# Kernel optimization log

Hardware: AMD Instinct MI355X
Metric: run time of the kernel (lower is better)

## Reference

```python
import jax, jax.numpy as jnp
import numpy as np

G = 256       # number of graphs in batch
NPG = 400     # nodes per graph (hardcoded in module)
DEG = 32      # avg degree
FIN = 400     # input feature dim
H = 64        # hidden_channels
N = G * NPG
E = G * NPG * DEG


def _glorot(key, fan_in, fan_out):
    lim = float(np.sqrt(6.0 / (fan_in + fan_out)))
    return jax.random.uniform(key, (fan_in, fan_out), jnp.float32, -lim, lim)


def setup_inputs() -> dict:
    key = jax.random.key(0)
    ks = jax.random.split(key, 12)
    x = jax.random.normal(ks[0], (N, FIN), jnp.float32)
    # intra-graph random edges, then offset by graph id so edges never cross graphs
    src = jax.random.randint(ks[1], (G, NPG * DEG), 0, NPG)
    dst = jax.random.randint(ks[2], (G, NPG * DEG), 0, NPG)
    offs = (jnp.arange(G) * NPG)[:, None]
    edge_index = jnp.stack([(src + offs).reshape(-1), (dst + offs).reshape(-1)]).astype(jnp.int32)
    edge_weight = jax.random.uniform(ks[3], (E,), jnp.float32)
    return {
        "x": x,
        "edge_index": edge_index,
        "edge_weight": edge_weight,
        "W1": _glorot(ks[4], FIN, H), "b1": jnp.zeros((H,), jnp.float32),
        "W2": _glorot(ks[5], H, H),   "b2": jnp.zeros((H,), jnp.float32),
        "W3": _glorot(ks[6], H, H),   "b3": jnp.zeros((H,), jnp.float32),
        "Wc": _glorot(ks[7], NPG * H, H), "bc": jnp.zeros((H,), jnp.float32),
        "Wl": _glorot(ks[8], H, 2),   "bl": jnp.zeros((2,), jnp.float32),
    }


def _gcn_conv(x, W, b, row, col, norm, n):
    # PyG GCNConv: out[col] += norm * (x @ W)[row]; then + bias
    h = x @ W                                   # [n, out]
    msg = norm[:, None] * h[row]                # [E+n, out] gather + scale
    return jax.ops.segment_sum(msg, col, num_segments=n) + b


def reference(x, edge_index, edge_weight, W1, b1, W2, b2, W3, b3, Wc, bc, Wl, bl):
    n = x.shape[0]
    loop = jnp.arange(n, dtype=edge_index.dtype)
    row = jnp.concatenate([edge_index[0], loop])            # sources (with self-loops)
    col = jnp.concatenate([edge_index[1], loop])            # targets
    ew = jnp.concatenate([edge_weight, jnp.ones((n,), edge_weight.dtype)])
    # symmetric normalization: deg^{-1/2}[row] * w * deg^{-1/2}[col]
    deg = jax.ops.segment_sum(ew, col, num_segments=n)
    dinv = jnp.where(deg > 0, jax.lax.rsqrt(deg), 0.0)
    norm = dinv[row] * ew * dinv[col]

    h = jax.nn.relu(_gcn_conv(x, W1, b1, row, col, norm, n))
    h = jax.nn.relu(_gcn_conv(h, W2, b2, row, col, norm, n))
    h = _gcn_conv(h, W3, b3, row, col, norm, n)
    # per-graph flatten of 400 nodes -> lincomb (vectorized form of the Python loop)
    g = h.reshape(-1, NPG * H) @ Wc + bc        # [G, H]
    # dropout p=0.5 skipped (eval mode)
    return g @ Wl + bl                          # [G, 2]
```

## Files before the change

### kernel.cpp

```cpp
#include <hip/hip_runtime.h>
#include <hip/hip_bf16.h>
#include <stdint.h>

#define G 256
#define NPG 400
#define DEG 32
#define FIN 400
#define H 64
#define NN (G*NPG)
#define EE (G*NPG*DEG)
#define EPG (NPG*DEG)
#define CPG (EPG+NPG)
#define NTILE 13
#define ATS 420
#define HTS 72
#define MTSZ 25600

#define W1F_OFF 0
#define W1F_N   (13*4*64*8)
#define W2F_OFF (W1F_OFF + W1F_N)
#define W2F_N   (2*4*64*8)
#define W3F_OFF (W2F_OFF + W2F_N)
#define WCF_OFF (W3F_OFF + W2F_N)
#define WCF_N   (800*4*64*8)
#define WF_TOT  (WCF_OFF + WCF_N)

typedef __attribute__((ext_vector_type(8))) _Float16 h8;
typedef __attribute__((ext_vector_type(4))) float f32x4;

static __device__ __forceinline__ unsigned packh2(float a, float b) {
  unsigned short ua = __builtin_bit_cast(unsigned short, (_Float16)a);
  unsigned short ub = __builtin_bit_cast(unsigned short, (_Float16)b);
  return (unsigned)ua | ((unsigned)ub << 16);
}

static __device__ __forceinline__ h8 cvt8(float4 a, float4 b) {
  h8 r;
  r[0] = (_Float16)a.x; r[1] = (_Float16)a.y; r[2] = (_Float16)a.z; r[3] = (_Float16)a.w;
  r[4] = (_Float16)b.x; r[5] = (_Float16)b.y; r[6] = (_Float16)b.z; r[7] = (_Float16)b.w;
  return r;
}

__global__ __launch_bounds__(256) void kNorm(
    const int* __restrict__ ei, const float* __restrict__ ew,
    uint2* __restrict__ ent, uint32_t* __restrict__ boff)
{
  __shared__ float deg[NPG];
  __shared__ float dv[NPG];
  __shared__ uint32_t bcnt[NTILE], bpos[NTILE];
  const int g = blockIdx.x, tid = threadIdx.x;
  const int ebase = g*EPG, nbase = g*NPG;
  const int* rowp = ei;
  const int* colp = ei + EE;
  if (tid < NTILE) bcnt[tid] = 0u;
  for (int v = tid; v < NPG; v += 256) deg[v] = 1.0f;
  __syncthreads();
  for (int e = tid; e < EPG; e += 256) {
    int c = colp[ebase+e] - nbase;
    atomicAdd(&deg[c], ew[ebase+e]);
    atomicAdd(&bcnt[c >> 5], 1u);
  }
  __syncthreads();
  for (int v = tid; v < NPG; v += 256) dv[v] = rsqrtf(deg[v]);
  if (tid == 0) {
    uint32_t s = 0;
    #pragma unroll
    for (int t = 0; t < NTILE; ++t) {
      uint32_t c = bcnt[t] + ((t < 12) ? 32u : 16u);
      bcnt[t] = s; bpos[t] = s; s += c;
    }
  }
  __syncthreads();
  if (tid < NTILE) boff[g*16 + tid] = bcnt[tid];
  if (tid == NTILE) boff[g*16 + NTILE] = (uint32_t)CPG;
  uint2* eb = ent + (size_t)g*CPG;
  for (int e = tid; e < EPG; e += 256) {
    int src = rowp[ebase+e] - nbase;
    int dst = colp[ebase+e] - nbase;
    float nm = dv[src] * ew[ebase+e] * dv[dst];
    uint32_t p = atomicAdd(&bpos[dst >> 5], 1u);
    eb[p] = make_uint2(((unsigned)dst << 16) | (unsigned)src, __float_as_uint(nm));
  }
  for (int v = tid; v < NPG; v += 256) {
    uint32_t p = atomicAdd(&bpos[v >> 5], 1u);
    eb[p] = make_uint2(((unsigned)v << 16) | (unsigned)v, __float_as_uint(dv[v]*dv[v]));
  }
}

__global__ __launch_bounds__(256) void kPack(
    const float* __restrict__ W1, const float* __restrict__ W2,
    const float* __restrict__ W3, const float* __restrict__ Wc,
    _Float16* __restrict__ wf, float* __restrict__ gbuf)
{
  int idx = blockIdx.x*256 + threadIdx.x;
  if (idx < G*H) gbuf[idx] = 0.f;
  if (idx >= WF_TOT) return;
  if (idx < W2F_OFF) {
    int i = idx;
    int j = i & 7, ln = (i >> 3) & 63, nt = (i >> 9) & 3, ks = i >> 11;
    int k = ks*32 + (ln >> 4)*8 + j, col = nt*16 + (ln & 15);
    wf[idx] = (k < FIN) ? (_Float16)W1[k*H + col] : (_Float16)0.f;
  } else if (idx < W3F_OFF) {
    int i = idx - W2F_OFF;
    int j = i & 7, ln = (i >> 3) & 63, nt = (i >> 9) & 3, ks = i >> 11;
    wf[idx] = (_Float16)W2[(ks*32 + (ln >> 4)*8 + j)*H + nt*16 + (ln & 15)];
  } else if (idx < WCF_OFF) {
    int i = idx - W3F_OFF;
    int j = i & 7, ln = (i >> 3) & 63, nt = (i >> 9) & 3, ks = i >> 11;
    wf[idx] = (_Float16)W3[(ks*32 + (ln >> 4)*8 + j)*H + nt*16 + (ln & 15)];
  } else {
    int i = idx - WCF_OFF;
    int j = i & 7, ln = (i >> 3) & 63, nt = (i >> 9) & 3, kt = i >> 11;
    int kp = kt*32 + (ln >> 4)*8 + j;
    int node = kp % 400, feat = kp / 400;
    int col = nt*16 + (ln & 15);
    wf[idx] = (_Float16)Wc[((size_t)node*64 + feat)*64 + col];
  }
}

__global__ __launch_bounds__(256, 4) void kM1(
    const float* __restrict__ x, const _Float16* __restrict__ wf,
    _Float16* __restrict__ mt1)
{
  __shared__ _Float16 sh[64*HTS];
  const int tid = threadIdx.x, lane = tid & 63, wave = tid >> 6;
  const int l15 = lane & 15, kgrp = lane >> 4;
  const int g = blockIdx.y, b = blockIdx.x;
  const int node_l = b*64 + wave*16 + l15;
  const int arow = (node_l < NPG) ? node_l : NPG-1;
  const float* xp = x + ((size_t)g*NPG + arow)*FIN;

  h8 af[13];
  #pragma unroll
  for (int ks = 0; ks < 13; ++ks) {
    int kb = ks*32 + kgrp*8;
    if (kb + 8 <= FIN) {
      float4 a0 = *(const float4*)(xp + kb);
      float4 a1 = *(const float4*)(xp + kb + 4);
      af[ks] = cvt8(a0, a1);
    } else {
      h8 z;
      #pragma unroll
      for (int j = 0; j < 8; ++j) z[j] = (_Float16)0.f;
      af[ks] = z;
    }
  }
  f32x4 acc[4] = {{0,0,0,0},{0,0,0,0},{0,0,0,0},{0,0,0,0}};
  for (int nt = 0; nt < 4; ++nt)
    for (int ks = 0; ks < 13; ++ks) {
      h8 bf = *(const h8*)&wf[W1F_OFF + (((size_t)ks*4 + nt)*64 + lane)*8];
      acc[nt] = __builtin_amdgcn_mfma_f32_16x16x32_f16(af[ks], bf, acc[nt], 0, 0, 0);
    }
  #pragma unroll
  for (int nt = 0; nt < 4; ++nt) {
    int feat = nt*16 + l15;
    #pragma unroll
    for (int r = 0; r < 4; ++r)
      sh[(wave*16 + kgrp*4 + r)*HTS + feat] = (_Float16)acc[nt][r];
  }
  __syncthreads();
  const unsigned short* shu = (const unsigned short*)sh;
  for (int i = tid; i < 64*16; i += 256) {
    int feat = i >> 4, seg = i & 15;
    int nl = seg*4, gn = b*64 + nl;
    if (gn < NPG) {
      uint2 u;
      u.x = (unsigned)shu[(nl+0)*HTS + feat] | ((unsigned)shu[(nl+1)*HTS + feat] << 16);
      u.y = (unsigned)shu[(nl+2)*HTS + feat] | ((unsigned)shu[(nl+3)*HTS + feat] << 16);
      *(uint2*)&mt1[(size_t)g*MTSZ + feat*400 + gn] = u;
    }
  }
}

template<int WMUL>
__global__ __launch_bounds__(512, 4) void kAgg(
    const _Float16* __restrict__ mtin, const _Float16* __restrict__ wfn,
    const float* __restrict__ bias,
    const uint2* __restrict__ ent, const uint32_t* __restrict__ boff,
    _Float16* __restrict__ out)
{
  extern __shared__ char smem[];
  float* sAT = (float*)smem;
  _Float16* sh = (_Float16*)(smem + 32*ATS*4);
  const int tid = threadIdx.x, lane = tid & 63, wave = tid >> 6;
  const int l15 = lane & 15, kgrp = lane >> 4;
  const int bid = blockIdx.x;
  const int g = bid & 255, t = bid >> 8;
  const int t0 = t*32;
  const int rsub = wave & 1, nt = wave >> 1;
  const uint2* eb = ent + (size_t)g*CPG;
  const uint32_t s0 = boff[g*16 + t], s1 = boff[g*16 + t + 1];

  h8 BF[13];
  const _Float16* mrow = mtin + (size_t)g*MTSZ + (nt*16 + l15)*400;
  #pragma unroll
  for (int ks = 0; ks < 13; ++ks)
    BF[ks] = *(const h8*)(mrow + ks*32 + kgrp*8);
  const float bv = bias[nt*16 + l15];
  h8 WF2[2];
  if (WMUL) {
    WF2[0] = *(const h8*)&wfn[((size_t)(0*4 + nt)*64 + lane)*8];
    WF2[1] = *(const h8*)&wfn[((size_t)(1*4 + nt)*64 + lane)*8];
  }
  const uint32_t e0 = s0 + tid;
  uint2 E0 = make_uint2(0,0), E1 = make_uint2(0,0), E2 = make_uint2(0,0);
  if (e0        < s1) E0 = eb[e0];
  if (e0 + 512  < s1) E1 = eb[e0 + 512];
  if (e0 + 1024 < s1) E2 = eb[e0 + 1024];

  { float4* p = (float4*)sAT;
    for (int i = tid; i < 32*ATS/4; i += 512) p[i] = make_float4(0,0,0,0); }
  __syncthreads();

  if (e0        < s1) atomicAdd(&sAT[((int)(E0.x >> 16) - t0)*ATS + (int)(E0.x & 0xffffu)], __uint_as_float(E0.y));
  if (e0 + 512  < s1) atomicAdd(&sAT[((int)(E1.x >> 16) - t0)*ATS + (int)(E1.x & 0xffffu)], __uint_as_float(E1.y));
  if (e0 + 1024 < s1) atomicAdd(&sAT[((int)(E2.x >> 16) - t0)*ATS + (int)(E2.x & 0xffffu)], __uint_as_float(E2.y));
  for (uint32_t e = e0 + 1536; e < s1; e += 512) {
    uint2 E = eb[e];
    atomicAdd(&sAT[((int)(E.x >> 16) - t0)*ATS + (int)(E.x & 0xffffu)], __uint_as_float(E.y));
  }
  __syncthreads();

  f32x4 acc = {0,0,0,0};
  const float* ap = &sAT[(rsub*16 + l15)*ATS];
  #pragma unroll
  for (int ks = 0; ks < 13; ++ks) {
    int kb = ks*32 + kgrp*8;
    float4 a0 = *(const float4*)(ap + kb);
    float4 a1 = *(const float4*)(ap + kb + 4);
    acc = __builtin_amdgcn_mfma_f32_16x16x32_f16(cvt8(a0, a1), BF[ks], acc, 0, 0, 0);
  }

  if (!WMUL) {
    int node0 = t0 + rsub*16 + kgrp*4;
    if (node0 < NPG) {
      uint2 u;
      u.x = packh2(acc[0] + bv, acc[1] + bv);
      u.y = packh2(acc[2] + bv, acc[3] + bv);
      *(uint2*)&out[(size_t)g*MTSZ + (nt*16 + l15)*400 + node0] = u;
    }
  } else {
    int nl0 = rsub*16 + kgrp*4;
    #pragma unroll
    for (int r = 0; r < 4; ++r)
      sh[(nl0 + r)*HTS + nt*16 + l15] = (_Float16)fmaxf(acc[r] + bv, 0.f);
    __syncthreads();
    f32x4 acc2 = {0,0,0,0};
    const _Float16* hp = &sh[(rsub*16 + l15)*HTS];
    acc2 = __builtin_amdgcn_mfma_f32_16x16x32_f16(*(const h8*)(hp + kgrp*8),      WF2[0], acc2, 0, 0, 0);
    acc2 = __builtin_amdgcn_mfma_f32_16x16x32_f16(*(const h8*)(hp + 32 + kgrp*8), WF2[1], acc2, 0, 0, 0);
    int node0 = t0 + rsub*16 + kgrp*4;
    if (node0 < NPG) {
      uint2 u;
      u.x = packh2(acc2[0], acc2[1]);
      u.y = packh2(acc2[2], acc2[3]);
      *(uint2*)&out[(size_t)g*MTSZ + (nt*16 + l15)*400 + node0] = u;
    }
  }
}

__global__ __launch_bounds__(256) void kRead(
    const _Float16* __restrict__ h3, const _Float16* __restrict__ wfc,
    float* __restrict__ gbuf)
{
  const int tid = threadIdx.x, lane = tid & 63, nt = tid >> 6;
  const int l15 = lane & 15, kgrp = lane >> 4;
  const int rt = blockIdx.x & 15, kc = blockIdx.x >> 4;
  f32x4 acc = {0,0,0,0};
  const _Float16* hp = h3 + (size_t)(rt*16 + l15)*MTSZ;
  for (int ks = 0; ks < 25; ++ks) {
    int kt = kc*25 + ks;
    h8 af = *(const h8*)(hp + kt*32 + kgrp*8);
    h8 bf = *(const h8*)(wfc + (((size_t)kt*4 + nt)*64 + lane)*8);
    acc = __builtin_amdgcn_mfma_f32_16x16x32_f16(af, bf, acc, 0, 0, 0);
  }
  #pragma unroll
  for (int r = 0; r < 4; ++r)
    atomicAdd(&gbuf[(size_t)(rt*16 + kgrp*4 + r)*H + nt*16 + l15], acc[r]);
}

__global__ __launch_bounds__(512) void k6_final(
    const float* __restrict__ gbuf, const float* __restrict__ bc,
    const float* __restrict__ Wl, const float* __restrict__ bl,
    float* __restrict__ out)
{
  int t = threadIdx.x;
  int gr = t >> 1, c = t & 1;
  float acc = bl[c];
  for (int f = 0; f < H; ++f)
    acc += (gbuf[gr*H + f] + bc[f]) * Wl[f*2 + c];
  out[gr*2 + c] = acc;
}

extern "C" void kernel_launch(void* const* d_in, const int* in_sizes, int n_in,
                              void* d_out, int out_size, void* d_ws, size_t ws_size,
                              hipStream_t stream)
{
  const float* x  = (const float*)d_in[0];
  const int*   ei = (const int*)d_in[1];
  const float* ew = (const float*)d_in[2];
  const float* W1 = (const float*)d_in[3];
  const float* b1 = (const float*)d_in[4];
  const float* W2 = (const float*)d_in[5];
  const float* b2 = (const float*)d_in[6];
  const float* W3 = (const float*)d_in[7];
  const float* b3 = (const float*)d_in[8];
  const float* Wc = (const float*)d_in[9];
  const float* bc = (const float*)d_in[10];
  const float* Wl = (const float*)d_in[11];
  const float* bl = (const float*)d_in[12];
  float* out = (float*)d_out;
  (void)ws_size;

  char* ws = (char*)d_ws;
  size_t o = 0;
  uint2*     ent  = (uint2*)(ws + o);     o += (size_t)G*CPG*8;
  uint32_t*  boff = (uint32_t*)(ws + o);  o += (size_t)G*16*4;
  _Float16*  mtA  = (_Float16*)(ws + o);  o += (size_t)G*MTSZ*2 + 256;
  _Float16*  mtB  = (_Float16*)(ws + o);  o += (size_t)G*MTSZ*2 + 256;
  _Float16*  wf   = (_Float16*)(ws + o);  o += (size_t)WF_TOT*2;
  float*     gbuf = (float*)(ws + o);     o += (size_t)G*H*4;

  kPack<<<(WF_TOT+255)/256, 256, 0, stream>>>(W1, W2, W3, Wc, wf, gbuf);
  kNorm<<<G, 256, 0, stream>>>(ei, ew, ent, boff);
  kM1<<<dim3(7, G), 256, 0, stream>>>(x, wf, mtA);
  const int aggLds = 32*ATS*4 + 32*HTS*2;
  kAgg<1><<<NTILE*G, 512, aggLds, stream>>>(mtA, wf + W2F_OFF, b1, ent, boff, mtB);
  kAgg<1><<<NTILE*G, 512, aggLds, stream>>>(mtB, wf + W3F_OFF, b2, ent, boff, mtA);
  kAgg<0><<<NTILE*G, 512, aggLds, stream>>>(mtA, wf, b3, ent, boff, mtB);
  kRead<<<512, 256, 0, stream>>>(mtB, wf + WCF_OFF, gbuf);
  k6_final<<<1, 512, 0, stream>>>(gbuf, bc, Wl, bl, out);
}
```

Baseline: 290.3 us.

## Merge front-end kernels into one launch and halve aggregation tile size

Merges the normalization/CSR-bucket build, the first-layer X·W1 MFMA GEMM, and the Wc repacking into one heterogeneous kFront launch whose blocks are split by index range. W1–W3 packing stays in a separate kernel. The aggregation kernels now use 16-node destination tiles (25 tiles per graph) with 256-thread blocks, doubling the block count and halving LDS per block, which should raise occupancy. The final projection is spread across 8 blocks. This removes launches and serial dependencies between the front-end kernels, but kFront's LDS is sized only for the M1 path (9216 B), while the norm path also uses about 3.4 KB, which fits.

Result: slower. 306.6 us (+5.6%).

```diff
diff --git a/kernel.cpp b/kernel.cpp
--- a/kernel.cpp
+++ b/kernel.cpp
@@ -11,7 +11,7 @@
 #define EE (G*NPG*DEG)
 #define EPG (NPG*DEG)
 #define CPG (EPG+NPG)
-#define NTILE 13
+#define NTILE 25
 #define ATS 420
 #define HTS 72
 #define MTSZ 25600
@@ -25,6 +25,10 @@
 #define WCF_N   (800*4*64*8)
 #define WF_TOT  (WCF_OFF + WCF_N)
 
+#define FB_M1   1792
+#define FB_NORM (FB_M1 + G)
+#define FB_WC   (FB_NORM + WCF_N/256)
+
 typedef __attribute__((ext_vector_type(8))) _Float16 h8;
 typedef __attribute__((ext_vector_type(4))) float f32x4;
 
@@ -41,60 +45,14 @@
   return r;
 }
 
-__global__ __launch_bounds__(256) void kNorm(
-    const int* __restrict__ ei, const float* __restrict__ ew,
-    uint2* __restrict__ ent, uint32_t* __restrict__ boff)
-{
-  __shared__ float deg[NPG];
-  __shared__ float dv[NPG];
-  __shared__ uint32_t bcnt[NTILE], bpos[NTILE];
-  const int g = blockIdx.x, tid = threadIdx.x;
-  const int ebase = g*EPG, nbase = g*NPG;
-  const int* rowp = ei;
-  const int* colp = ei + EE;
-  if (tid < NTILE) bcnt[tid] = 0u;
-  for (int v = tid; v < NPG; v += 256) deg[v] = 1.0f;
-  __syncthreads();
-  for (int e = tid; e < EPG; e += 256) {
-    int c = colp[ebase+e] - nbase;
-    atomicAdd(&deg[c], ew[ebase+e]);
-    atomicAdd(&bcnt[c >> 5], 1u);
-  }
-  __syncthreads();
-  for (int v = tid; v < NPG; v += 256) dv[v] = rsqrtf(deg[v]);
-  if (tid == 0) {
-    uint32_t s = 0;
-    #pragma unroll
-    for (int t = 0; t < NTILE; ++t) {
-      uint32_t c = bcnt[t] + ((t < 12) ? 32u : 16u);
-      bcnt[t] = s; bpos[t] = s; s += c;
-    }
-  }
-  __syncthreads();
-  if (tid < NTILE) boff[g*16 + tid] = bcnt[tid];
-  if (tid == NTILE) boff[g*16 + NTILE] = (uint32_t)CPG;
-  uint2* eb = ent + (size_t)g*CPG;
-  for (int e = tid; e < EPG; e += 256) {
-    int src = rowp[ebase+e] - nbase;
-    int dst = colp[ebase+e] - nbase;
-    float nm = dv[src] * ew[ebase+e] * dv[dst];
-    uint32_t p = atomicAdd(&bpos[dst >> 5], 1u);
-    eb[p] = make_uint2(((unsigned)dst << 16) | (unsigned)src, __float_as_uint(nm));
-  }
-  for (int v = tid; v < NPG; v += 256) {
-    uint32_t p = atomicAdd(&bpos[v >> 5], 1u);
-    eb[p] = make_uint2(((unsigned)v << 16) | (unsigned)v, __float_as_uint(dv[v]*dv[v]));
-  }
-}
-
-__global__ __launch_bounds__(256) void kPack(
+__global__ __launch_bounds__(256) void kPackW(
     const float* __restrict__ W1, const float* __restrict__ W2,
-    const float* __restrict__ W3, const float* __restrict__ Wc,
+    const float* __restrict__ W3,
     _Float16* __restrict__ wf, float* __restrict__ gbuf)
 {
   int idx = blockIdx.x*256 + threadIdx.x;
   if (idx < G*H) gbuf[idx] = 0.f;
-  if (idx >= WF_TOT) return;
+  if (idx >= WCF_OFF) return;
   if (idx < W2F_OFF) {
     int i = idx;
     int j = i & 7, ln = (i >> 3) & 63, nt = (i >> 9) & 3, ks = i >> 11;
@@ -104,76 +62,126 @@
     int i = idx - W2F_OFF;
     int j = i & 7, ln = (i >> 3) & 63, nt = (i >> 9) & 3, ks = i >> 11;
     wf[idx] = (_Float16)W2[(ks*32 + (ln >> 4)*8 + j)*H + nt*16 + (ln & 15)];
-  } else if (idx < WCF_OFF) {
+  } else {
     int i = idx - W3F_OFF;
     int j = i & 7, ln = (i >> 3) & 63, nt = (i >> 9) & 3, ks = i >> 11;
     wf[idx] = (_Float16)W3[(ks*32 + (ln >> 4)*8 + j)*H + nt*16 + (ln & 15)];
+  }
+}
+
+__global__ __launch_bounds__(256) void kFront(
+    const float* __restrict__ x, const int* __restrict__ ei,
+    const float* __restrict__ ew, const float* __restrict__ Wc,
+    const _Float16* __restrict__ wfr, _Float16* __restrict__ wfw,
+    uint2* __restrict__ ent, uint32_t* __restrict__ boff,
+    _Float16* __restrict__ mt1)
+{
+  extern __shared__ char smem[];
+  const int b = blockIdx.x, tid = threadIdx.x;
+
+  if (b < FB_M1) {
+    _Float16* sh = (_Float16*)smem;
+    const int lane = tid & 63, wave = tid >> 6;
+    const int l15 = lane & 15, kgrp = lane >> 4;
+    const int g = b / 7, bt = b % 7;
+    const int node_l = bt*64 + wave*16 + l15;
+    const int arow = (node_l < NPG) ? node_l : NPG-1;
+    const float* xp = x + ((size_t)g*NPG + arow)*FIN;
+
+    h8 af[13];
+    #pragma unroll
+    for (int ks = 0; ks < 13; ++ks) {
+      int kb = ks*32 + kgrp*8;
+      if (kb + 8 <= FIN) {
+        float4 a0 = *(const float4*)(xp + kb);
+        float4 a1 = *(const float4*)(xp + kb + 4);
+        af[ks] = cvt8(a0, a1);
+      } else {
+        h8 z;
+        #pragma unroll
+        for (int j = 0; j < 8; ++j) z[j] = (_Float16)0.f;
+        af[ks] = z;
+      }
+    }
+    f32x4 acc[4] = {{0,0,0,0},{0,0,0,0},{0,0,0,0},{0,0,0,0}};
+    for (int nt = 0; nt < 4; ++nt)
+      for (int ks = 0; ks < 13; ++ks) {
+        h8 bf = *(const h8*)&wfr[W1F_OFF + (((size_t)ks*4 + nt)*64 + lane)*8];
+        acc[nt] = __builtin_amdgcn_mfma_f32_16x16x32_f16(af[ks], bf, acc[nt], 0, 0, 0);
+      }
+    #pragma unroll
+    for (int nt = 0; nt < 4; ++nt) {
+      int feat = nt*16 + l15;
+      #pragma unroll
+      for (int r = 0; r < 4; ++r)
+        sh[(wave*16 + kgrp*4 + r)*HTS + feat] = (_Float16)acc[nt][r];
+    }
+    __syncthreads();
+    const unsigned short* shu = (const unsigned short*)sh;
+    for (int i = tid; i < 64*16; i += 256) {
+      int feat = i >> 4, seg = i & 15;
+      int nl = seg*4, gn = bt*64 + nl;
+      if (gn < NPG) {
+        uint2 u;
+        u.x = (unsigned)shu[(nl+0)*HTS + feat] | ((unsigned)shu[(nl+1)*HTS + feat] << 16);
+        u.y = (unsigned)shu[(nl+2)*HTS + feat] | ((unsigned)shu[(nl+3)*HTS + feat] << 16);
+        *(uint2*)&mt1[(size_t)g*MTSZ + feat*400 + gn] = u;
+      }
+    }
+  } else if (b < FB_NORM) {
+    float* deg = (float*)smem;
+    float* dv  = deg + NPG;
+    uint32_t* bcnt = (uint32_t*)(dv + NPG);
+    uint32_t* bpos = bcnt + 32;
+    const int g = b - FB_M1;
+    const int ebase = g*EPG, nbase = g*NPG;
+    const int* rowp = ei;
+    const int* colp = ei + EE;
+    if (tid < NTILE) bcnt[tid] = 0u;
+    for (int v = tid; v < NPG; v += 256) deg[v] = 1.0f;
+    __syncthreads();
+    for (int e = tid; e < EPG; e += 256) {
+      int c = colp[ebase+e] - nbase;
+      atomicAdd(&deg[c], ew[ebase+e]);
+      atomicAdd(&bcnt[c >> 4], 1u);
+    }
+    __syncthreads();
+    for (int v = tid; v < NPG; v += 256) dv[v] = rsqrtf(deg[v]);
+    if (tid == 0) {
+      uint32_t s = 0;
+      #pragma unroll
+      for (int t = 0; t < NTILE; ++t) {
+        uint32_t c = bcnt[t] + 16u;
+        bcnt[t] = s; bpos[t] = s; s += c;
+      }
+    }
+    __syncthreads();
+    if (tid < NTILE) boff[g*32 + tid] = bcnt[tid];
+    if (tid == NTILE) boff[g*32 + NTILE] = (uint32_t)CPG;
+    uint2* eb = ent + (size_t)g*CPG;
+    for (int e = tid; e < EPG; e += 256) {
+      int src = rowp[ebase+e] - nbase;
+      int dst = colp[ebase+e] - nbase;
+      float nm = dv[src] * ew[ebase+e] * dv[dst];
+      uint32_t p = atomicAdd(&bpos[dst >> 4], 1u);
+      eb[p] = make_uint2(((unsigned)dst << 16) | (unsigned)src, __float_as_uint(nm));
+    }
+    for (int v = tid; v < NPG; v += 256) {
+      uint32_t p = atomicAdd(&bpos[v >> 4], 1u);
+      eb[p] = make_uint2(((unsigned)v << 16) | (unsigned)v, __float_as_uint(dv[v]*dv[v]));
+    }
   } else {
-    int i = idx - WCF_OFF;
-    int j = i & 7, ln = (i >> 3) & 63, nt = (i >> 9) & 3, kt = i >> 11;
+    int idx = (b - FB_NORM)*256 + tid;
+    int j = idx & 7, ln = (idx >> 3) & 63, nt = (idx >> 9) & 3, kt = idx >> 11;
     int kp = kt*32 + (ln >> 4)*8 + j;
     int node = kp % 400, feat = kp / 400;
     int col = nt*16 + (ln & 15);
-    wf[idx] = (_Float16)Wc[((size_t)node*64 + feat)*64 + col];
-  }
-}
-
-__global__ __launch_bounds__(256, 4) void kM1(
-    const float* __restrict__ x, const _Float16* __restrict__ wf,
-    _Float16* __restrict__ mt1)
-{
-  __shared__ _Float16 sh[64*HTS];
-  const int tid = threadIdx.x, lane = tid & 63, wave = tid >> 6;
-  const int l15 = lane & 15, kgrp = lane >> 4;
-  const int g = blockIdx.y, b = blockIdx.x;
-  const int node_l = b*64 + wave*16 + l15;
-  const int arow = (node_l < NPG) ? node_l : NPG-1;
-  const float* xp = x + ((size_t)g*NPG + arow)*FIN;
-
-  h8 af[13];
-  #pragma unroll
-  for (int ks = 0; ks < 13; ++ks) {
-    int kb = ks*32 + kgrp*8;
-    if (kb + 8 <= FIN) {
-      float4 a0 = *(const float4*)(xp + kb);
-      float4 a1 = *(const float4*)(xp + kb + 4);
-      af[ks] = cvt8(a0, a1);
-    } else {
-      h8 z;
-      #pragma unroll
-      for (int j = 0; j < 8; ++j) z[j] = (_Float16)0.f;
-      af[ks] = z;
-    }
-  }
-  f32x4 acc[4] = {{0,0,0,0},{0,0,0,0},{0,0,0,0},{0,0,0,0}};
-  for (int nt = 0; nt < 4; ++nt)
-    for (int ks = 0; ks < 13; ++ks) {
-      h8 bf = *(const h8*)&wf[W1F_OFF + (((size_t)ks*4 + nt)*64 + lane)*8];
-      acc[nt] = __builtin_amdgcn_mfma_f32_16x16x32_f16(af[ks], bf, acc[nt], 0, 0, 0);
-    }
-  #pragma unroll
-  for (int nt = 0; nt < 4; ++nt) {
-    int feat = nt*16 + l15;
-    #pragma unroll
-    for (int r = 0; r < 4; ++r)
-      sh[(wave*16 + kgrp*4 + r)*HTS + feat] = (_Float16)acc[nt][r];
-  }
-  __syncthreads();
-  const unsigned short* shu = (const unsigned short*)sh;
-  for (int i = tid; i < 64*16; i += 256) {
-    int feat = i >> 4, seg = i & 15;
-    int nl = seg*4, gn = b*64 + nl;
-    if (gn < NPG) {
-      uint2 u;
-      u.x = (unsigned)shu[(nl+0)*HTS + feat] | ((unsigned)shu[(nl+1)*HTS + feat] << 16);
-      u.y = (unsigned)shu[(nl+2)*HTS + feat] | ((unsigned)shu[(nl+3)*HTS + feat] << 16);
-      *(uint2*)&mt1[(size_t)g*MTSZ + feat*400 + gn] = u;
-    }
+    wfw[WCF_OFF + idx] = (_Float16)Wc[((size_t)node*64 + feat)*64 + col];
   }
 }
 
 template<int WMUL>
-__global__ __launch_bounds__(512, 4) void kAgg(
+__global__ __launch_bounds__(256, 4) void kAgg(
     const _Float16* __restrict__ mtin, const _Float16* __restrict__ wfn,
     const float* __restrict__ bias,
     const uint2* __restrict__ ent, const uint32_t* __restrict__ boff,
@@ -181,15 +189,15 @@
 {
   extern __shared__ char smem[];
   float* sAT = (float*)smem;
-  _Float16* sh = (_Float16*)(smem + 32*ATS*4);
-  const int tid = threadIdx.x, lane = tid & 63, wave = tid >> 6;
+  _Float16* sh = (_Float16*)(smem + 16*ATS*4);
+  const int tid = threadIdx.x, lane = tid & 63;
   const int l15 = lane & 15, kgrp = lane >> 4;
   const int bid = blockIdx.x;
   const int g = bid & 255, t = bid >> 8;
-  const int t0 = t*32;
-  const int rsub = wave & 1, nt = wave >> 1;
+  const int t0 = t*16;
+  const int nt = tid >> 6;
   const uint2* eb = ent + (size_t)g*CPG;
-  const uint32_t s0 = boff[g*16 + t], s1 = boff[g*16 + t + 1];
+  const uint32_t s0 = boff[g*32 + t], s1 = boff[g*32 + t + 1];
 
   h8 BF[13];
   const _Float16* mrow = mtin + (size_t)g*MTSZ + (nt*16 + l15)*400;
@@ -204,25 +212,25 @@
   }
   const uint32_t e0 = s0 + tid;
   uint2 E0 = make_uint2(0,0), E1 = make_uint2(0,0), E2 = make_uint2(0,0);
-  if (e0        < s1) E0 = eb[e0];
-  if (e0 + 512  < s1) E1 = eb[e0 + 512];
-  if (e0 + 1024 < s1) E2 = eb[e0 + 1024];
+  if (e0       < s1) E0 = eb[e0];
+  if (e0 + 256 < s1) E1 = eb[e0 + 256];
+  if (e0 + 512 < s1) E2 = eb[e0 + 512];
 
   { float4* p = (float4*)sAT;
-    for (int i = tid; i < 32*ATS/4; i += 512) p[i] = make_float4(0,0,0,0); }
+    for (int i = tid; i < 16*ATS/4; i += 256) p[i] = make_float4(0,0,0,0); }
   __syncthreads();
 
-  if (e0        < s1) atomicAdd(&sAT[((int)(E0.x >> 16) - t0)*ATS + (int)(E0.x & 0xffffu)], __uint_as_float(E0.y));
-  if (e0 + 512  < s1) atomicAdd(&sAT[((int)(E1.x >> 16) - t0)*ATS + (int)(E1.x & 0xffffu)], __uint_as_float(E1.y));
-  if (e0 + 1024 < s1) atomicAdd(&sAT[((int)(E2.x >> 16) - t0)*ATS + (int)(E2.x & 0xffffu)], __uint_as_float(E2.y));
-  for (uint32_t e = e0 + 1536; e < s1; e += 512) {
+  if (e0       < s1) atomicAdd(&sAT[((int)(E0.x >> 16) - t0)*ATS + (int)(E0.x & 0xffffu)], __uint_as_float(E0.y));
+  if (e0 + 256 < s1) atomicAdd(&sAT[((int)(E1.x >> 16) - t0)*ATS + (int)(E1.x & 0xffffu)], __uint_as_float(E1.y));
+  if (e0 + 512 < s1) atomicAdd(&sAT[((int)(E2.x >> 16) - t0)*ATS + (int)(E2.x & 0xffffu)], __uint_as_float(E2.y));
+  for (uint32_t e = e0 + 768; e < s1; e += 256) {
     uint2 E = eb[e];
     atomicAdd(&sAT[((int)(E.x >> 16) - t0)*ATS + (int)(E.x & 0xffffu)], __uint_as_float(E.y));
   }
   __syncthreads();
 
   f32x4 acc = {0,0,0,0};
-  const float* ap = &sAT[(rsub*16 + l15)*ATS];
+  const float* ap = &sAT[l15*ATS];
   #pragma unroll
   for (int ks = 0; ks < 13; ++ks) {
     int kb = ks*32 + kgrp*8;
@@ -231,31 +239,25 @@
     acc = __builtin_amdgcn_mfma_f32_16x16x32_f16(cvt8(a0, a1), BF[ks], acc, 0, 0, 0);
   }
 
+  const int node0 = t0 + kgrp*4;
   if (!WMUL) {
-    int node0 = t0 + rsub*16 + kgrp*4;
-    if (node0 < NPG) {
-      uint2 u;
-      u.x = packh2(acc[0] + bv, acc[1] + bv);
-      u.y = packh2(acc[2] + bv, acc[3] + bv);
-      *(uint2*)&out[(size_t)g*MTSZ + (nt*16 + l15)*400 + node0] = u;
-    }
+    uint2 u;
+    u.x = packh2(acc[0] + bv, acc[1] + bv);
+    u.y = packh2(acc[2] + bv, acc[3] + bv);
+    *(uint2*)&out[(size_t)g*MTSZ + (nt*16 + l15)*400 + node0] = u;
   } else {
-    int nl0 = rsub*16 + kgrp*4;
     #pragma unroll
     for (int r = 0; r < 4; ++r)
-      sh[(nl0 + r)*HTS + nt*16 + l15] = (_Float16)fmaxf(acc[r] + bv, 0.f);
+      sh[(kgrp*4 + r)*HTS + nt*16 + l15] = (_Float16)fmaxf(acc[r] + bv, 0.f);
     __syncthreads();
     f32x4 acc2 = {0,0,0,0};
-    const _Float16* hp = &sh[(rsub*16 + l15)*HTS];
+    const _Float16* hp = &sh[l15*HTS];
     acc2 = __builtin_amdgcn_mfma_f32_16x16x32_f16(*(const h8*)(hp + kgrp*8),      WF2[0], acc2, 0, 0, 0);
     acc2 = __builtin_amdgcn_mfma_f32_16x16x32_f16(*(const h8*)(hp + 32 + kgrp*8), WF2[1], acc2, 0, 0, 0);
-    int node0 = t0 + rsub*16 + kgrp*4;
-    if (node0 < NPG) {
-      uint2 u;
-      u.x = packh2(acc2[0], acc2[1]);
-      u.y = packh2(acc2[2], acc2[3]);
-      *(uint2*)&out[(size_t)g*MTSZ + (nt*16 + l15)*400 + node0] = u;
-    }
+    uint2 u;
+    u.x = packh2(acc2[0], acc2[1]);
+    u.y = packh2(acc2[2], acc2[3]);
+    *(uint2*)&out[(size_t)g*MTSZ + (nt*16 + l15)*400 + node0] = u;
   }
 }
 
@@ -279,12 +281,12 @@
     atomicAdd(&gbuf[(size_t)(rt*16 + kgrp*4 + r)*H + nt*16 + l15], acc[r]);
 }
 
-__global__ __launch_bounds__(512) void k6_final(
+__global__ __launch_bounds__(64) void k6_final(
     const float* __restrict__ gbuf, const float* __restrict__ bc,
     const float* __restrict__ Wl, const float* __restrict__ bl,
     float* __restrict__ out)
 {
-  int t = threadIdx.x;
+  int t = blockIdx.x*64 + threadIdx.x;
   int gr = t >> 1, c = t & 1;
   float acc = bl[c];
   for (int f = 0; f < H; ++f)
@@ -315,19 +317,18 @@
   char* ws = (char*)d_ws;
   size_t o = 0;
   uint2*     ent  = (uint2*)(ws + o);     o += (size_t)G*CPG*8;
-  uint32_t*  boff = (uint32_t*)(ws + o);  o += (size_t)G*16*4;
+  uint32_t*  boff = (uint32_t*)(ws + o);  o += (size_t)G*32*4;
   _Float16*  mtA  = (_Float16*)(ws + o);  o += (size_t)G*MTSZ*2 + 256;
   _Float16*  mtB  = (_Float16*)(ws + o);  o += (size_t)G*MTSZ*2 + 256;
   _Float16*  wf   = (_Float16*)(ws + o);  o += (size_t)WF_TOT*2;
   float*     gbuf = (float*)(ws + o);     o += (size_t)G*H*4;
 
-  kPack<<<(WF_TOT+255)/256, 256, 0, stream>>>(W1, W2, W3, Wc, wf, gbuf);
-  kNorm<<<G, 256, 0, stream>>>(ei, ew, ent, boff);
-  kM1<<<dim3(7, G), 256, 0, stream>>>(x, wf, mtA);
-  const int aggLds = 32*ATS*4 + 32*HTS*2;
-  kAgg<1><<<NTILE*G, 512, aggLds, stream>>>(mtA, wf + W2F_OFF, b1, ent, boff, mtB);
-  kAgg<1><<<NTILE*G, 512, aggLds, stream>>>(mtB, wf + W3F_OFF, b2, ent, boff, mtA);
-  kAgg<0><<<NTILE*G, 512, aggLds, stream>>>(mtA, wf, b3, ent, boff, mtB);
+  kPackW<<<(WCF_OFF+255)/256, 256, 0, stream>>>(W1, W2, W3, wf, gbuf);
+  kFront<<<FB_WC, 256, 64*HTS*2, stream>>>(x, ei, ew, Wc, wf, wf, ent, boff, mtA);
+  const int aggLds = 16*ATS*4 + 16*HTS*2;
+  kAgg<1><<<NTILE*G, 256, aggLds, stream>>>(mtA, wf + W2F_OFF, b1, ent, boff, mtB);
+  kAgg<1><<<NTILE*G, 256, aggLds, stream>>>(mtB, wf + W3F_OFF, b2, ent, boff, mtA);
+  kAgg<0><<<NTILE*G, 256, aggLds, stream>>>(mtA, wf, b3, ent, boff, mtB);
   kRead<<<512, 256, 0, stream>>>(mtB, wf + WCF_OFF, gbuf);
-  k6_final<<<1, 512, 0, stream>>>(gbuf, bc, Wl, bl, out);
-}
+  k6_final<<<8, 64, 0, stream>>>(gbuf, bc, Wl, bl, out);
+}
```
